# Performance work log

Hardware: AMD Instinct MI355X
Metric: run time of the kernel (lower is better)

## Reference

```python
import jax, jax.numpy as jnp
import numpy as np

B, S, E, H, D = 1, 2048, 1024, 16, 64
LAM_INIT = 0.8  # \u03bbinit from init_kwargs
LN_EPS = 1e-5


def setup_inputs() -> dict:
    key = jax.random.key(0)
    ks = jax.random.split(key, 6)
    w = 0.02  # weight init scale
    return {
        "X": jax.random.normal(ks[0], (B, S, E), dtype=jnp.float32),
        "Wq": jax.random.normal(ks[1], (H, E, 2 * D), dtype=jnp.float32) * w,
        "bq": jnp.zeros((H, 2 * D), dtype=jnp.float32),
        "Wk": jax.random.normal(ks[2], (H, E, 2 * D), dtype=jnp.float32) * w,
        "bk": jnp.zeros((H, 2 * D), dtype=jnp.float32),
        "Wv": jax.random.normal(ks[3], (H, E, D), dtype=jnp.float32) * w,
        "bv": jnp.zeros((H, D), dtype=jnp.float32),
        "Wo": jax.random.normal(ks[4], (H * D, E), dtype=jnp.float32) * w,
        "bo": jnp.zeros((E,), dtype=jnp.float32),
        "gamma": jnp.ones((E,), dtype=jnp.float32),
        "beta": jnp.zeros((E,), dtype=jnp.float32),
        "lam": jnp.float32(0.5),
    }


def reference(X, Wq, bq, Wk, bk, Wv, bv, Wo, bo, gamma, beta, lam):
    # Batched over heads: Q,K -> [B,H,S,2D], V -> [B,H,S,D]
    Q = jnp.einsum("bse,hec->bhsc", X, Wq) + bq[None, :, None, :]
    K = jnp.einsum("bse,hec->bhsc", X, Wk) + bk[None, :, None, :]
    V = jnp.einsum("bse,hed->bhsd", X, Wv) + bv[None, :, None, :]
    d = Wv.shape[-1]
    Q1, Q2 = Q[..., :d], Q[..., d:]
    K1, K2 = K[..., :d], K[..., d:]
    s = 1.0 / jnp.sqrt(jnp.float32(d))
    A1 = jnp.einsum("bhqd,bhkd->bhqk", Q1, K1) * s
    A2 = jnp.einsum("bhqd,bhkd->bhqk", Q2, K2) * s
    P = jax.nn.softmax(A1, axis=-1) - lam * jax.nn.softmax(A2, axis=-1)
    O = jnp.einsum("bhqk,bhkd->bhqd", P, V)  # [B,H,S,D]
    Ocat = jnp.transpose(O, (0, 2, 1, 3)).reshape(O.shape[0], O.shape[2], -1)  # [B,S,H*D]
    Y = Ocat @ Wo + bo
    mu = jnp.mean(Y, axis=-1, keepdims=True)
    var = jnp.var(Y, axis=-1, keepdims=True)
    Yn = (Y - mu) * jax.lax.rsqrt(var + LN_EPS) * gamma + beta
    return Yn * (1.0 - LAM_INIT)
```

## Files before the change

kernel.cpp:

```cpp
#include <hip/hip_runtime.h>

#define S_LEN 2048
#define EDIM  1024
#define HEADS 16
#define DHEAD 64

typedef __attribute__((ext_vector_type(8))) short bf16x8;
typedef __attribute__((ext_vector_type(4))) short short4v;
typedef __attribute__((ext_vector_type(4))) float f32x4;

__device__ inline unsigned short f2bf(float f) {
    unsigned int u = __float_as_uint(f);
    unsigned int r = (u + 0x7FFFu + ((u >> 16) & 1u)) >> 16;
    return (unsigned short)r;
}
__device__ inline float bf2f(unsigned short b) {
    return __uint_as_float(((unsigned int)b) << 16);
}
__device__ inline void load_lds16(const void* g, void* l) {
    __builtin_amdgcn_global_load_lds(
        (const __attribute__((address_space(1))) unsigned int*)g,
        (__attribute__((address_space(3))) unsigned int*)l, 16, 0, 0);
}

__global__ void k_convert_x(const float* __restrict__ x, short* __restrict__ xb, int n4) {
    int i = blockIdx.x * blockDim.x + threadIdx.x;
    if (i >= n4) return;
    f32x4 v = ((const f32x4*)x)[i];
    short4v o;
    o[0] = (short)f2bf(v[0]); o[1] = (short)f2bf(v[1]);
    o[2] = (short)f2bf(v[2]); o[3] = (short)f2bf(v[3]);
    ((short4v*)xb)[i] = o;
}

__global__ void k_transpose_cvt(const float* __restrict__ in, short* __restrict__ out, int R, int C) {
    __shared__ float tile[32][33];
    const int b = blockIdx.z;
    in  += (size_t)b * R * C;
    out += (size_t)b * R * C;
    const int c0 = blockIdx.x * 32, r0 = blockIdx.y * 32;
    #pragma unroll
    for (int yy = 0; yy < 4; ++yy) {
        int r = r0 + threadIdx.y + yy * 8, c = c0 + threadIdx.x;
        tile[threadIdx.y + yy * 8][threadIdx.x] = (r < R && c < C) ? in[(size_t)r * C + c] : 0.f;
    }
    __syncthreads();
    #pragma unroll
    for (int yy = 0; yy < 4; ++yy) {
        int c = c0 + threadIdx.y + yy * 8, r = r0 + threadIdx.x;
        if (c < C && r < R) out[(size_t)c * R + r] = (short)f2bf(tile[threadIdx.x][threadIdx.y + yy * 8]);
    }
}

template<int BM, int BN, int WR, int WC>
__device__ inline void gemm_core(const char* Ag, int ldaB, const char* Bg, int ldbB,
                                 int K, char* sA, char* sB, f32x4* acc) {
    constexpr int FM = BM / (WR * 16), FN = BN / (WC * 16);
    constexpr int RA = BM / 32, RB = BN / 32;
    const int lane = threadIdx.x & 63, wave = threadIdx.x >> 6;
    const int rl = lane & 15, g = lane >> 4;
    const int wrow = (wave / WC) * (BM / WR);
    const int wcol = (wave % WC) * (BN / WC);
    const int lr = lane >> 3;
    const int lc = ((lane & 7) ^ lr) << 4;
    const char* aSrc = Ag + (size_t)(wave * 8 + lr) * ldaB + lc;
    const char* bSrc = Bg + (size_t)(wave * 8 + lr) * ldbB + lc;

    for (int t = 0; t < K / 64; ++t) {
        __syncthreads();
        #pragma unroll
        for (int i = 0; i < RA; ++i)
            load_lds16(aSrc + (size_t)t * 128 + (size_t)i * 32 * ldaB, sA + (i * 4 + wave) * 1024);
        #pragma unroll
        for (int i = 0; i < RB; ++i)
            load_lds16(bSrc + (size_t)t * 128 + (size_t)i * 32 * ldbB, sB + (i * 4 + wave) * 1024);
        __syncthreads();
        #pragma unroll
        for (int kk = 0; kk < 2; ++kk) {
            bf16x8 af[FM], bf[FN];
            #pragma unroll
            for (int f = 0; f < FM; ++f) {
                const int r = wrow + f * 16 + rl;
                af[f] = *(const bf16x8*)(sA + r * 128 + (((kk * 4 + g) ^ (r & 7)) << 4));
            }
            #pragma unroll
            for (int j = 0; j < FN; ++j) {
                const int r = wcol + j * 16 + rl;
                bf[j] = *(const bf16x8*)(sB + r * 128 + (((kk * 4 + g) ^ (r & 7)) << 4));
            }
            #pragma unroll
            for (int f = 0; f < FM; ++f)
                #pragma unroll
                for (int j = 0; j < FN; ++j)
                    acc[f * FN + j] = __builtin_amdgcn_mfma_f32_16x16x32_bf16(af[f], bf[j], acc[f * FN + j], 0, 0, 0);
        }
    }
}

__global__ __launch_bounds__(256) void k_gemm_qkv(
        const short* __restrict__ Xb,
        const short* __restrict__ WqT, const short* __restrict__ WkT, const short* __restrict__ WvT,
        const float* __restrict__ bq, const float* __restrict__ bk, const float* __restrict__ bv,
        short* __restrict__ Qh, short* __restrict__ Kh, short* __restrict__ Vt) {
    __shared__ __align__(16) char sA[16384], sB[16384];
    int id = blockIdx.x;
    id = (id & 7) * 80 + (id >> 3);
    const int mbase = (id % 16) * 128;
    const int y = id / 16;

    const short* Bt; const float* bias; int nbase; int which;
    if (y < 16)      { which = 0; Bt = WqT; bias = bq; nbase = y * 128; }
    else if (y < 32) { which = 1; Bt = WkT; bias = bk; nbase = (y - 16) * 128; }
    else             { which = 2; Bt = WvT; bias = bv; nbase = (y - 32) * 128; }

    f32x4 acc[16];
    #pragma unroll
    for (int i = 0; i < 16; ++i) acc[i] = (f32x4){0.f, 0.f, 0.f, 0.f};

    gemm_core<128, 128, 2, 2>((const char*)Xb + (size_t)mbase * 2048, 2048,
                              (const char*)Bt + (size_t)nbase * 2048, 2048,
                              EDIM, sA, sB, acc);

    const int lane = threadIdx.x & 63, wave = threadIdx.x >> 6;
    const int wr = (wave >> 1) * 64, wc = (wave & 1) * 64;
    const int rl = lane & 15, g = lane >> 4;
    const float qscale = 0.125f * 1.44269504088896f;
    #pragma unroll
    for (int i = 0; i < 4; ++i)
        #pragma unroll
        for (int j = 0; j < 4; ++j)
            #pragma unroll
            for (int jj = 0; jj < 4; ++jj) {
                int s = mbase + wr + i * 16 + g * 4 + jj;
                int n = nbase + wc + j * 16 + rl;
                float v = acc[i * 4 + j][jj] + bias[n];
                if (which == 0) v *= qscale;
                short b16 = (short)f2bf(v);
                if (which == 0)      Qh[((size_t)(n >> 7) * S_LEN + s) * 128 + (n & 127)] = b16;
                else if (which == 1) Kh[((size_t)(n >> 7) * S_LEN + s) * 128 + (n & 127)] = b16;
                else                 Vt[(size_t)n * S_LEN + s] = b16;
            }
}

__global__ __launch_bounds__(512, 4) void k_attn(
        const short* __restrict__ Qh, const short* __restrict__ Kh,
        const short* __restrict__ Vt, const float* __restrict__ lam_p,
        short* __restrict__ Ocat) {
    __shared__ __align__(16) char smem[65536];

    const int lane = threadIdx.x & 63, wave = threadIdx.x >> 6;
    const int rl = lane & 15, g = lane >> 4;
    const int qw = wave & 3, kvg = wave >> 2;
    const int h = blockIdx.y;
    const int qbase = blockIdx.x * 64 + qw * 16;
    const int swz = (rl & 7) << 4;
    const int kx = rl & 7;

    char* Kl = smem + kvg * 16384;
    char* Vl = smem + 32768 + kvg * 8192;
    char* Pw = smem + 49152 + wave * 2048;

    const char* Kgb = (const char*)(Kh + (size_t)h * S_LEN * 128);
    const char* Vgb = (const char*)(Vt + (size_t)h * DHEAD * S_LEN);
    const short* Qp = Qh + (size_t)h * S_LEN * 128;

    const int kofs0 = (lane >> 4) * 256 + (((lane & 15) ^ (lane >> 4)) << 4);
    const int kofs1 = (lane >> 4) * 256 + (((lane & 15) ^ ((lane >> 4) + 4)) << 4);
    const int vofs  = (lane >> 3) * 4096 + (((lane & 7) ^ (lane >> 3)) << 4);

    bf16x8 qf[2][2];
    #pragma unroll
    for (int p = 0; p < 2; ++p)
        #pragma unroll
        for (int kc = 0; kc < 2; ++kc)
            qf[p][kc] = *(const bf16x8*)&Qp[(size_t)(qbase + rl) * 128 + p * 64 + kc * 32 + g * 8];

    f32x4 acc[2][4];
    float m[2], l[2];
    #pragma unroll
    for (int p = 0; p < 2; ++p) {
        #pragma unroll
        for (int t = 0; t < 4; ++t) acc[p][t] = (f32x4){0.f, 0.f, 0.f, 0.f};
        m[p] = 0.f; l[p] = 0.f;
    }

    const int NIT = 1024 / 64;
    for (int it = 0; it < NIT; ++it) {
        const size_t kv0 = (size_t)(kvg * 1024 + it * 64);
        __syncthreads();
        #pragma unroll
        for (int cc = 0; cc < 4; ++cc) {
            int c = qw * 4 + cc;
            load_lds16(Kgb + kv0 * 256 + c * 1024 + ((cc & 1) ? kofs1 : kofs0), Kl + c * 1024);
        }
        #pragma unroll
        for (int cc = 0; cc < 2; ++cc) {
            int c = qw * 2 + cc;
            load_lds16(Vgb + (size_t)c * 32768 + kv0 * 2 + vofs, Vl + c * 1024);
        }
        __syncthreads();

        #pragma unroll
        for (int p = 0; p < 2; ++p) {
            f32x4 sc[4];
            #pragma unroll
            for (int t = 0; t < 4; ++t) {
                f32x4 z = (f32x4){0.f, 0.f, 0.f, 0.f};
                #pragma unroll
                for (int kc = 0; kc < 2; ++kc) {
                    bf16x8 kf = *(const bf16x8*)(Kl + t * 4096 + rl * 256 + (((p * 8 + kc * 4 + g) ^ kx) << 4));
                    z = __builtin_amdgcn_mfma_f32_16x16x32_bf16(kf, qf[p][kc], z, 0, 0, 0);
                }
                sc[t] = z;
            }

            float mx = sc[0][0];
            #pragma unroll
            for (int t = 0; t < 4; ++t)
                #pragma unroll
                for (int jj = 0; jj < 4; ++jj)
                    mx = fmaxf(mx, sc[t][jj]);
            mx = fmaxf(mx, __shfl_xor(mx, 16, 64));
            mx = fmaxf(mx, __shfl_xor(mx, 32, 64));

            if (it == 0) {
                m[p] = mx;
            } else if (!__all(mx <= m[p] + 8.f)) {
                float mn = fmaxf(m[p], mx);
                float fac = exp2f(m[p] - mn);
                l[p] *= fac; m[p] = mn;
                #pragma unroll
                for (int jj = 0; jj < 4; ++jj) {
                    float fq = __shfl(fac, g * 4 + jj, 64);
                    #pragma unroll
                    for (int t = 0; t < 4; ++t) acc[p][t][jj] *= fq;
                }
            }

            float rs = 0.f;
            #pragma unroll
            for (int t = 0; t < 4; ++t) {
                #pragma unroll
                for (int jjp = 0; jjp < 4; jjp += 2) {
                    float e0 = exp2f(sc[t][jjp]     - m[p]);
                    float e1 = exp2f(sc[t][jjp + 1] - m[p]);
                    rs += e0 + e1;
                    unsigned u;
                    asm("v_cvt_pk_bf16_f32 %0, %1, %2" : "=v"(u) : "v"(e0), "v"(e1));
                    *(unsigned*)(Pw + rl * 128 + (((t * 16 + g * 4 + jjp) * 2) ^ swz)) = u;
                }
            }
            rs += __shfl_xor(rs, 16, 64);
            rs += __shfl_xor(rs, 32, 64);
            l[p] += rs;

            #pragma unroll
            for (int kc = 0; kc < 2; ++kc) {
                bf16x8 pa = *(const bf16x8*)(Pw + rl * 128 + ((kc * 64 + g * 16) ^ swz));
                #pragma unroll
                for (int t = 0; t < 4; ++t) {
                    bf16x8 vf = *(const bf16x8*)(Vl + t * 2048 + rl * 128 + (((kc * 4 + g) ^ kx) << 4));
                    acc[p][t] = __builtin_amdgcn_mfma_f32_16x16x32_bf16(pa, vf, acc[p][t], 0, 0, 0);
                }
            }
        }
    }

    __syncthreads();
    {
        unsigned short* Xw = (unsigned short*)(smem + wave * 4096);
        float* ML = (float*)(smem + 32768);
        #pragma unroll
        for (int p = 0; p < 2; ++p) {
            #pragma unroll
            for (int t = 0; t < 4; ++t)
                #pragma unroll
                for (int jj = 0; jj < 4; ++jj)
                    Xw[p * 1024 + (g * 4 + jj) * 64 + t * 16 + rl] = f2bf(acc[p][t][jj]);
            if (g == 0) {
                ML[(wave * 2 + p) * 32 + rl]      = m[p];
                ML[(wave * 2 + p) * 32 + 16 + rl] = l[p];
            }
        }
    }
    __syncthreads();

    {
        const int q = threadIdx.x >> 3, d0 = (threadIdx.x & 7) * 8;
        const int q15 = q & 15, wa = q >> 4, wb = (q >> 4) + 4;
        const float* ML = (const float*)(smem + 32768);
        const float lam = lam_p[0];
        float res[2][8];
        float invL[2];
        #pragma unroll
        for (int p = 0; p < 2; ++p) {
            float ma = ML[(wa * 2 + p) * 32 + q15], la = ML[(wa * 2 + p) * 32 + 16 + q15];
            float mb = ML[(wb * 2 + p) * 32 + q15], lb = ML[(wb * 2 + p) * 32 + 16 + q15];
            float ms = fmaxf(ma, mb);
            float fa = exp2f(ma - ms), fb = exp2f(mb - ms);
            invL[p] = 1.0f / (fa * la + fb * lb);
            const unsigned short* xa = (const unsigned short*)(smem + wa * 4096 + p * 2048 + q15 * 128 + d0 * 2);
            const unsigned short* xb = (const unsigned short*)(smem + wb * 4096 + p * 2048 + q15 * 128 + d0 * 2);
            #pragma unroll
            for (int k = 0; k < 8; ++k)
                res[p][k] = fa * bf2f(xa[k]) + fb * bf2f(xb[k]);
        }
        bf16x8 ov;
        #pragma unroll
        for (int k = 0; k < 8; ++k)
            ov[k] = (short)f2bf(res[0][k] * invL[0] - lam * res[1][k] * invL[1]);
        *(bf16x8*)&Ocat[(size_t)(blockIdx.x * 64 + q) * 1024 + h * 64 + d0] = ov;
    }
}

__global__ __launch_bounds__(256) void k_gemm_out(
        const short* __restrict__ Ocat, const short* __restrict__ WoT,
        const float* __restrict__ bo, float* __restrict__ Yws) {
    __shared__ __align__(16) char sA[8192], sB[16384];
    int id = blockIdx.x;
    id = (id & 7) * 32 + (id >> 3);
    const int mbase = (id % 32) * 64;
    const int nbase = (id / 32) * 128;

    f32x4 acc[8];
    #pragma unroll
    for (int i = 0; i < 8; ++i) acc[i] = (f32x4){0.f, 0.f, 0.f, 0.f};

    gemm_core<64, 128, 1, 4>((const char*)Ocat + (size_t)mbase * 2048, 2048,
                             (const char*)WoT + (size_t)nbase * 2048, 2048,
                             1024, sA, sB, acc);

    const int lane = threadIdx.x & 63, wave = threadIdx.x >> 6;
    const int rl = lane & 15, g = lane >> 4;
    #pragma unroll
    for (int f = 0; f < 4; ++f)
        #pragma unroll
        for (int j = 0; j < 2; ++j)
            #pragma unroll
            for (int jj = 0; jj < 4; ++jj) {
                int s = mbase + f * 16 + g * 4 + jj;
                int e = nbase + wave * 32 + j * 16 + rl;
                Yws[(size_t)s * 1024 + e] = acc[f * 2 + j][jj] + bo[e];
            }
}

__global__ __launch_bounds__(256) void k_ln(
        const float* __restrict__ Yws, const float* __restrict__ gamma,
        const float* __restrict__ beta, float* __restrict__ out) {
    const int s = blockIdx.x;
    const int tid = threadIdx.x;
    f32x4 y = ((const f32x4*)(Yws + (size_t)s * 1024))[tid];
    float sum = y[0] + y[1] + y[2] + y[3];
    float sq  = y[0]*y[0] + y[1]*y[1] + y[2]*y[2] + y[3]*y[3];
    #pragma unroll
    for (int off = 1; off < 64; off <<= 1) {
        sum += __shfl_xor(sum, off, 64);
        sq  += __shfl_xor(sq,  off, 64);
    }
    __shared__ float ls[2][4];
    const int wave = tid >> 6, lane = tid & 63;
    if (lane == 0) { ls[0][wave] = sum; ls[1][wave] = sq; }
    __syncthreads();
    sum = ls[0][0] + ls[0][1] + ls[0][2] + ls[0][3];
    sq  = ls[1][0] + ls[1][1] + ls[1][2] + ls[1][3];
    const float mu = sum * (1.f / 1024.f);
    const float var = sq * (1.f / 1024.f) - mu * mu;
    const float rstd = rsqrtf(var + 1e-5f);
    f32x4 gg = ((const f32x4*)gamma)[tid];
    f32x4 bb = ((const f32x4*)beta)[tid];
    f32x4 o;
    #pragma unroll
    for (int k = 0; k < 4; ++k)
        o[k] = ((y[k] - mu) * rstd * gg[k] + bb[k]) * 0.2f;
    ((f32x4*)(out + (size_t)s * 1024))[tid] = o;
}

extern "C" void kernel_launch(void* const* d_in, const int* in_sizes, int n_in,
                              void* d_out, int out_size, void* d_ws, size_t ws_size,
                              hipStream_t stream) {
    const float* X     = (const float*)d_in[0];
    const float* Wq    = (const float*)d_in[1];
    const float* bq    = (const float*)d_in[2];
    const float* Wk    = (const float*)d_in[3];
    const float* bk    = (const float*)d_in[4];
    const float* Wv    = (const float*)d_in[5];
    const float* bv    = (const float*)d_in[6];
    const float* Wo    = (const float*)d_in[7];
    const float* bo    = (const float*)d_in[8];
    const float* gamma = (const float*)d_in[9];
    const float* beta  = (const float*)d_in[10];
    const float* lam   = (const float*)d_in[11];
    float* out = (float*)d_out;

    char* ws = (char*)d_ws;
    const size_t MB = 1u << 20;
    short* Xb  = (short*)(ws + 0);
    short* WqT = (short*)(ws + 4 * MB);
    short* WkT = (short*)(ws + 8 * MB);
    short* WvT = (short*)(ws + 12 * MB);
    short* WoT = (short*)(ws + 14 * MB);
    short* Qh  = (short*)(ws + 16 * MB);
    short* Kh  = (short*)(ws + 24 * MB);
    short* Vt  = (short*)(ws + 32 * MB);
    short* Oc  = (short*)(ws + 36 * MB);
    float* Yws = (float*)(ws + 0);

    k_convert_x<<<dim3(2048), dim3(256), 0, stream>>>(X, Xb, (S_LEN * EDIM) / 4);
    k_transpose_cvt<<<dim3(4, 32, 16), dim3(32, 8), 0, stream>>>(Wq, WqT, 1024, 128);
    k_transpose_cvt<<<dim3(4, 32, 16), dim3(32, 8), 0, stream>>>(Wk, WkT, 1024, 128);
    k_transpose_cvt<<<dim3(2, 32, 16), dim3(32, 8), 0, stream>>>(Wv, WvT, 1024, 64);
    k_transpose_cvt<<<dim3(32, 32, 1), dim3(32, 8), 0, stream>>>(Wo, WoT, 1024, 1024);
    k_gemm_qkv<<<dim3(640), dim3(256), 0, stream>>>(Xb, WqT, WkT, WvT, bq, bk, bv, Qh, Kh, Vt);
    k_attn<<<dim3(32, 16), dim3(512), 0, stream>>>(Qh, Kh, Vt, lam, Oc);
    k_gemm_out<<<dim3(256), dim3(256), 0, stream>>>(Oc, WoT, bo, Yws);
    k_ln<<<dim3(2048), dim3(256), 0, stream>>>(Yws, gamma, beta, out);
}
```

Baseline: 173.1 us.

## Double-buffer K/V tiles in attention and drop split-KV cross-wave merge

The attention kernel no longer splits the key range between two wave groups. Each of the 8 waves now owns 16 query rows over the full 2048-key sequence, and K/V tiles are double-buffered in LDS so the next tile's global-to-LDS load overlaps compute on the current one. This removes the end-of-kernel LDS merge of partial softmax stats and outputs and writes Ocat directly from registers. The trade-off is half as many blocks (256 instead of 512), twice as many loop iterations per block, and a lower launch-bounds occupancy hint.

```diff
diff --git a/kernel.cpp b/kernel.cpp
--- a/kernel.cpp
+++ b/kernel.cpp
@@ -142,7 +142,7 @@
             }
 }
 
-__global__ __launch_bounds__(512, 4) void k_attn(
+__global__ __launch_bounds__(512, 2) void k_attn(
         const short* __restrict__ Qh, const short* __restrict__ Kh,
         const short* __restrict__ Vt, const float* __restrict__ lam_p,
         short* __restrict__ Ocat) {
@@ -150,14 +150,11 @@
 
     const int lane = threadIdx.x & 63, wave = threadIdx.x >> 6;
     const int rl = lane & 15, g = lane >> 4;
-    const int qw = wave & 3, kvg = wave >> 2;
     const int h = blockIdx.y;
-    const int qbase = blockIdx.x * 64 + qw * 16;
+    const int qbase = blockIdx.x * 128 + wave * 16;
     const int swz = (rl & 7) << 4;
     const int kx = rl & 7;
 
-    char* Kl = smem + kvg * 16384;
-    char* Vl = smem + 32768 + kvg * 8192;
     char* Pw = smem + 49152 + wave * 2048;
 
     const char* Kgb = (const char*)(Kh + (size_t)h * S_LEN * 128);
@@ -168,6 +165,20 @@
     const int kofs1 = (lane >> 4) * 256 + (((lane & 15) ^ ((lane >> 4) + 4)) << 4);
     const int vofs  = (lane >> 3) * 4096 + (((lane & 7) ^ (lane >> 3)) << 4);
 
+    auto STAGE = [&](int b, int it) {
+        const size_t kv0 = (size_t)it * 64;
+        char* kb = smem + b * 16384;
+        char* vb = smem + 32768 + b * 8192;
+        #pragma unroll
+        for (int cc = 0; cc < 2; ++cc) {
+            int c = wave * 2 + cc;
+            load_lds16(Kgb + kv0 * 256 + c * 1024 + ((c & 1) ? kofs1 : kofs0), kb + c * 1024);
+        }
+        load_lds16(Vgb + (size_t)wave * 32768 + kv0 * 2 + vofs, vb + wave * 1024);
+    };
+
+    STAGE(0, 0);
+
     bf16x8 qf[2][2];
     #pragma unroll
     for (int p = 0; p < 2; ++p)
@@ -184,21 +195,14 @@
         m[p] = 0.f; l[p] = 0.f;
     }
 
-    const int NIT = 1024 / 64;
+    __syncthreads();
+
+    const int NIT = S_LEN / 64;
     for (int it = 0; it < NIT; ++it) {
-        const size_t kv0 = (size_t)(kvg * 1024 + it * 64);
-        __syncthreads();
-        #pragma unroll
-        for (int cc = 0; cc < 4; ++cc) {
-            int c = qw * 4 + cc;
-            load_lds16(Kgb + kv0 * 256 + c * 1024 + ((cc & 1) ? kofs1 : kofs0), Kl + c * 1024);
-        }
-        #pragma unroll
-        for (int cc = 0; cc < 2; ++cc) {
-            int c = qw * 2 + cc;
-            load_lds16(Vgb + (size_t)c * 32768 + kv0 * 2 + vofs, Vl + c * 1024);
-        }
-        __syncthreads();
+        const int cur = it & 1;
+        if (it + 1 < NIT) STAGE(cur ^ 1, it + 1);
+        const char* Kl = smem + cur * 16384;
+        const char* Vl = smem + 32768 + cur * 8192;
 
         #pragma unroll
         for (int p = 0; p < 2; ++p) {
@@ -264,53 +268,24 @@
                 }
             }
         }
-    }
-
-    __syncthreads();
-    {
-        unsigned short* Xw = (unsigned short*)(smem + wave * 4096);
-        float* ML = (float*)(smem + 32768);
-        #pragma unroll
-        for (int p = 0; p < 2; ++p) {
-            #pragma unroll
-            for (int t = 0; t < 4; ++t)
-                #pragma unroll
-                for (int jj = 0; jj < 4; ++jj)
-                    Xw[p * 1024 + (g * 4 + jj) * 64 + t * 16 + rl] = f2bf(acc[p][t][jj]);
-            if (g == 0) {
-                ML[(wave * 2 + p) * 32 + rl]      = m[p];
-                ML[(wave * 2 + p) * 32 + 16 + rl] = l[p];
-            }
+        __syncthreads();
+    }
+
+    const float lam = lam_p[0];
+    float inv0[4], inv1[4];
+    #pragma unroll
+    for (int jj = 0; jj < 4; ++jj) {
+        inv0[jj] = 1.0f / __shfl(l[0], g * 4 + jj, 64);
+        inv1[jj] = lam  / __shfl(l[1], g * 4 + jj, 64);
+    }
+    #pragma unroll
+    for (int t = 0; t < 4; ++t)
+        #pragma unroll
+        for (int jj = 0; jj < 4; ++jj) {
+            float o = acc[0][t][jj] * inv0[jj] - acc[1][t][jj] * inv1[jj];
+            int s = qbase + g * 4 + jj;
+            Ocat[(size_t)s * 1024 + h * 64 + t * 16 + rl] = (short)f2bf(o);
         }
-    }
-    __syncthreads();
-
-    {
-        const int q = threadIdx.x >> 3, d0 = (threadIdx.x & 7) * 8;
-        const int q15 = q & 15, wa = q >> 4, wb = (q >> 4) + 4;
-        const float* ML = (const float*)(smem + 32768);
-        const float lam = lam_p[0];
-        float res[2][8];
-        float invL[2];
-        #pragma unroll
-        for (int p = 0; p < 2; ++p) {
-            float ma = ML[(wa * 2 + p) * 32 + q15], la = ML[(wa * 2 + p) * 32 + 16 + q15];
-            float mb = ML[(wb * 2 + p) * 32 + q15], lb = ML[(wb * 2 + p) * 32 + 16 + q15];
-            float ms = fmaxf(ma, mb);
-            float fa = exp2f(ma - ms), fb = exp2f(mb - ms);
-            invL[p] = 1.0f / (fa * la + fb * lb);
-            const unsigned short* xa = (const unsigned short*)(smem + wa * 4096 + p * 2048 + q15 * 128 + d0 * 2);
-            const unsigned short* xb = (const unsigned short*)(smem + wb * 4096 + p * 2048 + q15 * 128 + d0 * 2);
-            #pragma unroll
-            for (int k = 0; k < 8; ++k)
-                res[p][k] = fa * bf2f(xa[k]) + fb * bf2f(xb[k]);
-        }
-        bf16x8 ov;
-        #pragma unroll
-        for (int k = 0; k < 8; ++k)
-            ov[k] = (short)f2bf(res[0][k] * invL[0] - lam * res[1][k] * invL[1]);
-        *(bf16x8*)&Ocat[(size_t)(blockIdx.x * 64 + q) * 1024 + h * 64 + d0] = ov;
-    }
 }
 
 __global__ __launch_bounds__(256) void k_gemm_out(
@@ -411,7 +386,7 @@
     k_transpose_cvt<<<dim3(2, 32, 16), dim3(32, 8), 0, stream>>>(Wv, WvT, 1024, 64);
     k_transpose_cvt<<<dim3(32, 32, 1), dim3(32, 8), 0, stream>>>(Wo, WoT, 1024, 1024);
     k_gemm_qkv<<<dim3(640), dim3(256), 0, stream>>>(Xb, WqT, WkT, WvT, bq, bk, bv, Qh, Kh, Vt);
-    k_attn<<<dim3(32, 16), dim3(512), 0, stream>>>(Qh, Kh, Vt, lam, Oc);
+    k_attn<<<dim3(16, 16), dim3(512), 0, stream>>>(Qh, Kh, Vt, lam, Oc);
     k_gemm_out<<<dim3(256), dim3(256), 0, stream>>>(Oc, WoT, bo, Yws);
     k_ln<<<dim3(2048), dim3(256), 0, stream>>>(Yws, gamma, beta, out);
 }
```

New measurement: 181.1 us. 1.05x slower.

## Double-buffer K/V tiles in attention loop with 32-key steps

Applied to the files above, without the earlier changes.

Splits each KV group's LDS region into two half-size buffers and prefetches the next 32-key tile while computing the current one. This removes one of the two barriers per iteration and overlaps global-to-LDS loads with MFMA work. The tile size halves, so the loop runs twice as many iterations with smaller per-iteration MFMA batches, and the P and V swizzles are reworked to match. It also adds more online-softmax max/rescale checks per key.

```diff
diff --git a/kernel.cpp b/kernel.cpp
--- a/kernel.cpp
+++ b/kernel.cpp
@@ -153,20 +153,32 @@
     const int qw = wave & 3, kvg = wave >> 2;
     const int h = blockIdx.y;
     const int qbase = blockIdx.x * 64 + qw * 16;
-    const int swz = (rl & 7) << 4;
     const int kx = rl & 7;
-
-    char* Kl = smem + kvg * 16384;
-    char* Vl = smem + 32768 + kvg * 8192;
-    char* Pw = smem + 49152 + wave * 2048;
+    const int px = (rl & 3) << 4;
+
+    char* Kg0 = smem + kvg * 16384;
+    char* Vg0 = smem + 32768 + kvg * 8192;
+    char* Pw  = smem + 49152 + wave * 2048;
 
     const char* Kgb = (const char*)(Kh + (size_t)h * S_LEN * 128);
     const char* Vgb = (const char*)(Vt + (size_t)h * DHEAD * S_LEN);
     const short* Qp = Qh + (size_t)h * S_LEN * 128;
 
+    const int kc0 = qw * 2, kc1 = qw * 2 + 1;
     const int kofs0 = (lane >> 4) * 256 + (((lane & 15) ^ (lane >> 4)) << 4);
     const int kofs1 = (lane >> 4) * 256 + (((lane & 15) ^ ((lane >> 4) + 4)) << 4);
-    const int vofs  = (lane >> 3) * 4096 + (((lane & 7) ^ (lane >> 3)) << 4);
+    const int vofs  = (lane >> 2) * 4096 + (((lane & 3) ^ ((lane >> 2) & 3)) << 4);
+
+    auto STAGE = [&](int b, int it) {
+        const size_t kv0 = (size_t)(kvg * 1024 + it * 32);
+        char* kb = Kg0 + b * 8192;
+        char* vb = Vg0 + b * 4096;
+        load_lds16(Kgb + (kv0 + (size_t)kc0 * 4) * 256 + kofs0, kb + kc0 * 1024);
+        load_lds16(Kgb + (kv0 + (size_t)kc1 * 4) * 256 + kofs1, kb + kc1 * 1024);
+        load_lds16(Vgb + (size_t)(qw * 16) * 4096 + kv0 * 2 + vofs, vb + qw * 1024);
+    };
+
+    STAGE(0, 0);
 
     bf16x8 qf[2][2];
     #pragma unroll
@@ -184,31 +196,24 @@
         m[p] = 0.f; l[p] = 0.f;
     }
 
-    const int NIT = 1024 / 64;
+    __syncthreads();
+
+    const int NIT = 1024 / 32;
     for (int it = 0; it < NIT; ++it) {
-        const size_t kv0 = (size_t)(kvg * 1024 + it * 64);
-        __syncthreads();
-        #pragma unroll
-        for (int cc = 0; cc < 4; ++cc) {
-            int c = qw * 4 + cc;
-            load_lds16(Kgb + kv0 * 256 + c * 1024 + ((cc & 1) ? kofs1 : kofs0), Kl + c * 1024);
-        }
-        #pragma unroll
-        for (int cc = 0; cc < 2; ++cc) {
-            int c = qw * 2 + cc;
-            load_lds16(Vgb + (size_t)c * 32768 + kv0 * 2 + vofs, Vl + c * 1024);
-        }
-        __syncthreads();
+        const int cur = it & 1;
+        if (it + 1 < NIT) STAGE(cur ^ 1, it + 1);
+        const char* kb = Kg0 + cur * 8192;
+        const char* vb = Vg0 + cur * 4096;
 
         #pragma unroll
         for (int p = 0; p < 2; ++p) {
-            f32x4 sc[4];
-            #pragma unroll
-            for (int t = 0; t < 4; ++t) {
+            f32x4 sc[2];
+            #pragma unroll
+            for (int t = 0; t < 2; ++t) {
                 f32x4 z = (f32x4){0.f, 0.f, 0.f, 0.f};
                 #pragma unroll
                 for (int kc = 0; kc < 2; ++kc) {
-                    bf16x8 kf = *(const bf16x8*)(Kl + t * 4096 + rl * 256 + (((p * 8 + kc * 4 + g) ^ kx) << 4));
+                    bf16x8 kf = *(const bf16x8*)(kb + t * 4096 + rl * 256 + (((p * 8 + kc * 4 + g) ^ kx) << 4));
                     z = __builtin_amdgcn_mfma_f32_16x16x32_bf16(kf, qf[p][kc], z, 0, 0, 0);
                 }
                 sc[t] = z;
@@ -216,7 +221,7 @@
 
             float mx = sc[0][0];
             #pragma unroll
-            for (int t = 0; t < 4; ++t)
+            for (int t = 0; t < 2; ++t)
                 #pragma unroll
                 for (int jj = 0; jj < 4; ++jj)
                     mx = fmaxf(mx, sc[t][jj]);
@@ -239,7 +244,7 @@
 
             float rs = 0.f;
             #pragma unroll
-            for (int t = 0; t < 4; ++t) {
+            for (int t = 0; t < 2; ++t) {
                 #pragma unroll
                 for (int jjp = 0; jjp < 4; jjp += 2) {
                     float e0 = exp2f(sc[t][jjp]     - m[p]);
@@ -247,26 +252,23 @@
                     rs += e0 + e1;
                     unsigned u;
                     asm("v_cvt_pk_bf16_f32 %0, %1, %2" : "=v"(u) : "v"(e0), "v"(e1));
-                    *(unsigned*)(Pw + rl * 128 + (((t * 16 + g * 4 + jjp) * 2) ^ swz)) = u;
+                    *(unsigned*)(Pw + p * 1024 + rl * 64 + (((t * 16 + g * 4 + jjp) * 2) ^ px)) = u;
                 }
             }
             rs += __shfl_xor(rs, 16, 64);
             rs += __shfl_xor(rs, 32, 64);
             l[p] += rs;
 
-            #pragma unroll
-            for (int kc = 0; kc < 2; ++kc) {
-                bf16x8 pa = *(const bf16x8*)(Pw + rl * 128 + ((kc * 64 + g * 16) ^ swz));
-                #pragma unroll
-                for (int t = 0; t < 4; ++t) {
-                    bf16x8 vf = *(const bf16x8*)(Vl + t * 2048 + rl * 128 + (((kc * 4 + g) ^ kx) << 4));
-                    acc[p][t] = __builtin_amdgcn_mfma_f32_16x16x32_bf16(pa, vf, acc[p][t], 0, 0, 0);
-                }
+            bf16x8 pa = *(const bf16x8*)(Pw + p * 1024 + rl * 64 + ((g * 16) ^ px));
+            #pragma unroll
+            for (int t = 0; t < 4; ++t) {
+                bf16x8 vf = *(const bf16x8*)(vb + (t * 16 + rl) * 64 + (((g) ^ (rl & 3)) << 4));
+                acc[p][t] = __builtin_amdgcn_mfma_f32_16x16x32_bf16(pa, vf, acc[p][t], 0, 0, 0);
             }
         }
-    }
-
-    __syncthreads();
+        __syncthreads();
+    }
+
     {
         unsigned short* Xw = (unsigned short*)(smem + wave * 4096);
         float* ML = (float*)(smem + 32768);
```

Result: slower. 179.4 us (+3.6%).
